# Kernel optimization log

Measured on AMD Instinct MI355X. Metric: run time of the kernel, lower is better.

## Reference

```python
import jax, jax.numpy as jnp
import numpy as np

V, E, H, L, S, B, FE = 50257, 768, 12, 4, 1024, 2, 4
HD = E // H
EPS = 1e-5


def setup_inputs() -> dict:
    key = jax.random.key(0)
    ks = jax.random.split(key, 16)
    def n(k, shape, scale=0.02):
        return jax.random.normal(k, shape, jnp.float32) * scale
    x = jax.random.randint(ks[0], (B, S), 0, V)
    mask = jnp.tril(jnp.ones((S, S), jnp.int32))[None, None]  # (1,1,S,S) causal
    return {
        "x": x,
        "mask": mask,
        "embed_W": n(ks[1], (V, E)),
        "pos_embed": n(ks[2], (1, S, E)),
        "fc_out_W": n(ks[3], (L, E, E)),
        "fc_out_b": jnp.zeros((L, E), jnp.float32),
        "gate_W": n(ks[4], (L, E, E)),
        "gate_b": jnp.zeros((L, E), jnp.float32),
        "ln1_g": jnp.ones((L, E), jnp.float32),
        "ln1_b": jnp.zeros((L, E), jnp.float32),
        "ln2_g": jnp.ones((L, E), jnp.float32),
        "ln2_b": jnp.zeros((L, E), jnp.float32),
        "ff1_W": n(ks[5], (L, E, FE * E)),
        "ff1_b": jnp.zeros((L, FE * E), jnp.float32),
        "ff2_W": n(ks[6], (L, FE * E, E)),
        "ff2_b": jnp.zeros((L, E), jnp.float32),
        "lnf_g": jnp.ones((E,), jnp.float32),
        "lnf_b": jnp.zeros((E,), jnp.float32),
        "head_W": n(ks[7], (E, V)),
    }


def _layernorm(y, g, b):
    m = jnp.mean(y, -1, keepdims=True)
    v = jnp.mean((y - m) ** 2, -1, keepdims=True)
    return (y - m) * jax.lax.rsqrt(v + EPS) * g + b


def reference(x, mask, embed_W, pos_embed, fc_out_W, fc_out_b, gate_W, gate_b,
              ln1_g, ln1_b, ln2_g, ln2_b, ff1_W, ff1_b, ff2_W, ff2_b,
              lnf_g, lnf_b, head_W):
    h = embed_W[x] + pos_embed[:, :x.shape[1], :]  # (B,S,E)
    scale = 1.0 / np.sqrt(HD)
    for i in range(L):
        # NOTE: source never applies the q/k/v Linear layers; heads are split directly.
        q = h.reshape(B, S, H, HD).transpose(0, 2, 1, 3)  # (B,H,S,HD)
        energy = jnp.einsum('bhqd,bhkd->bhqk', q, q)
        energy = jnp.where(mask == 0, jnp.float32(-1e20), energy)
        attn = jax.nn.softmax(energy * scale, axis=-1)
        o = jnp.einsum('bhqk,bhkd->bhqd', attn, q)
        o = o.transpose(0, 2, 1, 3).reshape(B, S, E)
        o = o @ fc_out_W[i] + fc_out_b[i]
        gate = jax.nn.sigmoid(jnp.mean(h, 1, keepdims=True) @ gate_W[i] + gate_b[i])
        h = _layernorm(gate * o + h, ln1_g[i], ln1_b[i])
        ff = jax.nn.gelu(h @ ff1_W[i] + ff1_b[i], approximate=False) @ ff2_W[i] + ff2_b[i]
        h = _layernorm(ff + h, ln2_g[i], ln2_b[i])
    h = _layernorm(h, lnf_g, lnf_b)
    logits = h @ head_W  # (B,S,V)
    return logits
```

## Files before the change

### kernel.cpp

```cpp
#include <hip/hip_runtime.h>
#include <hip/hip_bf16.h>

#define V 50257
#define E 768
#define NH 12
#define NL 4
#define SS 1024
#define BB 2
#define FEE 4
#define HD 64
#define EPSL 1e-5f
#define NPADH 50432

typedef __hip_bfloat16 bf16;
typedef __attribute__((ext_vector_type(8))) short short8;
typedef __attribute__((ext_vector_type(4))) float f32x4;
typedef __attribute__((ext_vector_type(4), aligned(4))) float f32x4a;

#define GLD_SRC(p) (const __attribute__((address_space(1))) void*)(p)
#define GLD_DST(p) (__attribute__((address_space(3))) void*)(p)

__device__ __forceinline__ float b2f(bf16 x){ return __bfloat162float(x); }

__global__ __launch_bounds__(256) void embed_kernel(const int* __restrict__ x, const float* __restrict__ eW,
                                                    const float* __restrict__ pos, bf16* __restrict__ hb){
  size_t i = (size_t)blockIdx.x*256 + threadIdx.x;
  if (i >= (size_t)BB*SS*E) return;
  int e = (int)(i % E);
  size_t bs = i / E;
  int s = (int)(bs % SS);
  int tok = x[bs];
  hb[i] = __float2bfloat16(eW[(size_t)tok*E + e] + pos[(size_t)s*E + e]);
}

__global__ __launch_bounds__(256) void cvt_attn(const bf16* __restrict__ hb, bf16* __restrict__ vT){
  __shared__ short t[64][65];
  int bid = blockIdx.x;
  int st = bid & 15, hh = (bid >> 4) % NH, b = bid / (16*NH);
  int s0 = st*64;
  int c = threadIdx.x & 63, rr = threadIdx.x >> 6;
  #pragma unroll
  for (int i = 0; i < 16; ++i){
    int r = rr*16 + i;
    t[r][c] = __builtin_bit_cast(short, hb[(size_t)(b*SS + s0 + r)*E + hh*HD + c]);
  }
  __syncthreads();
  #pragma unroll
  for (int i = 0; i < 16; ++i){
    int d = rr*16 + i;
    vT[(size_t)((b*NH + hh)*HD + d)*SS + s0 + c] = __builtin_bit_cast(bf16, t[c][d]);
  }
}

__global__ __launch_bounds__(256) void attn_mfma(const bf16* __restrict__ hb, const bf16* __restrict__ vT,
                                                 bf16* __restrict__ Ab){
  __shared__ short Qs[64*64];
  __shared__ short Ks[128*64];
  __shared__ short Vs[64*128];
  __shared__ short Ps[4][16*128];
  int tid = threadIdx.x, wave = tid >> 6, lane = tid & 63;
  int bid = blockIdx.x;
  int qt = 15 - (bid & 15);
  int hh = (bid >> 4) % NH, b = bid / (16*NH);
  int q0 = qt*64;
  int l15 = lane & 15, l4 = lane >> 4;
  int sw7 = l15 & 7;

  #pragma unroll
  for (int rnd = 0; rnd < 2; ++rnd){
    int o = rnd*256 + tid; int row = o >> 3; int cs = (((o & 7) ^ (row & 7))*8);
    __builtin_amdgcn_global_load_lds(GLD_SRC(hb + ((size_t)(b*SS + q0 + row)*E + hh*HD + cs)),
                                     GLD_DST(Qs + o*8), 16, 0, 0);
  }

  float mrun[4], lrun[4];
  #pragma unroll
  for (int j = 0; j < 4; ++j){ mrun[j] = -1e30f; lrun[j] = 0.f; }
  f32x4 acco[4] = {};

  int nkt = (qt >> 1) + 1;
  for (int kt = 0; kt < nkt; ++kt){
    int k0 = kt*128;
    __syncthreads();
    #pragma unroll
    for (int rnd = 0; rnd < 4; ++rnd){
      int o = rnd*256 + tid; int row = o >> 3; int cs = (((o & 7) ^ (row & 7))*8);
      __builtin_amdgcn_global_load_lds(GLD_SRC(hb + ((size_t)(b*SS + k0 + row)*E + hh*HD + cs)),
                                       GLD_DST(Ks + o*8), 16, 0, 0);
    }
    #pragma unroll
    for (int rnd = 0; rnd < 4; ++rnd){
      int o = rnd*256 + tid; int row = o >> 4; int cs = (((o & 15) ^ (row & 15))*8);
      __builtin_amdgcn_global_load_lds(GLD_SRC(vT + ((size_t)((b*NH + hh)*HD + row)*SS + k0 + cs)),
                                       GLD_DST(Vs + o*8), 16, 0, 0);
    }
    __syncthreads();

    f32x4 s[8] = {};
    __builtin_amdgcn_s_setprio(1);
    #pragma unroll
    for (int kk = 0; kk < 2; ++kk){
      int slot = kk*4 + l4;
      short8 af = *(const short8*)&Qs[(wave*16 + l15)*64 + ((slot ^ sw7)*8)];
      #pragma unroll
      for (int n = 0; n < 8; ++n){
        short8 bf8 = *(const short8*)&Ks[(n*16 + l15)*64 + ((slot ^ sw7)*8)];
        s[n] = __builtin_amdgcn_mfma_f32_16x16x32_bf16(af, bf8, s[n], 0, 0, 0);
      }
    }
    __builtin_amdgcn_s_setprio(0);

    bool diag = (kt == nkt - 1);
    #pragma unroll
    for (int j = 0; j < 4; ++j){
      int qg = q0 + wave*16 + l4*4 + j;
      float tmax = -1e30f;
      #pragma unroll
      for (int n = 0; n < 8; ++n){
        float v = s[n][j]*0.125f;
        if (diag && (k0 + n*16 + l15) > qg) v = -1e30f;
        s[n][j] = v; tmax = fmaxf(tmax, v);
      }
      tmax = fmaxf(tmax, __shfl_xor(tmax, 1, 64));
      tmax = fmaxf(tmax, __shfl_xor(tmax, 2, 64));
      tmax = fmaxf(tmax, __shfl_xor(tmax, 4, 64));
      tmax = fmaxf(tmax, __shfl_xor(tmax, 8, 64));
      float mnew = fmaxf(mrun[j], tmax);
      float alpha = __expf(mrun[j] - mnew);
      float rsum = 0.f;
      #pragma unroll
      for (int n = 0; n < 8; ++n){
        float p = __expf(s[n][j] - mnew);
        s[n][j] = p; rsum += p;
      }
      rsum += __shfl_xor(rsum, 1, 64);
      rsum += __shfl_xor(rsum, 2, 64);
      rsum += __shfl_xor(rsum, 4, 64);
      rsum += __shfl_xor(rsum, 8, 64);
      lrun[j] = lrun[j]*alpha + rsum;
      mrun[j] = mnew;
      #pragma unroll
      for (int n = 0; n < 4; ++n) acco[n][j] *= alpha;
      int prow = l4*4 + j;
      #pragma unroll
      for (int n = 0; n < 8; ++n){
        bf16 hv = __float2bfloat16(s[n][j]);
        int slot = (n*2 + (l15 >> 3)) ^ prow;
        Ps[wave][prow*128 + slot*8 + (l15 & 7)] = __builtin_bit_cast(short, hv);
      }
    }
    __syncthreads();

    __builtin_amdgcn_s_setprio(1);
    #pragma unroll
    for (int kk = 0; kk < 4; ++kk){
      int slot = kk*4 + l4;
      short8 pa = *(const short8*)&Ps[wave][l15*128 + ((slot ^ l15)*8)];
      #pragma unroll
      for (int n = 0; n < 4; ++n){
        short8 vb = *(const short8*)&Vs[(n*16 + l15)*128 + ((slot ^ l15)*8)];
        acco[n] = __builtin_amdgcn_mfma_f32_16x16x32_bf16(pa, vb, acco[n], 0, 0, 0);
      }
    }
    __builtin_amdgcn_s_setprio(0);
  }

  #pragma unroll
  for (int j = 0; j < 4; ++j){
    float inv = 1.f / lrun[j];
    int qg = q0 + wave*16 + l4*4 + j;
    #pragma unroll
    for (int n = 0; n < 4; ++n){
      Ab[(size_t)(b*SS + qg)*E + hh*HD + n*16 + l15] = __float2bfloat16(acco[n][j]*inv);
    }
  }
}

__global__ __launch_bounds__(256) void hmean1_kernel(const bf16* __restrict__ hb, float* __restrict__ ph){
  int bid = blockIdx.x;
  int ec = bid % 3, tc = (bid/3) & 15, b = bid / 48;
  int e = ec*256 + threadIdx.x;
  float s = 0.f;
  #pragma unroll 8
  for (int t = tc*64; t < tc*64 + 64; ++t) s += b2f(hb[((size_t)b*SS + t)*E + e]);
  ph[((size_t)b*16 + tc)*E + e] = s;
}

__global__ __launch_bounds__(256) void gate1_kernel(const float* __restrict__ ph, const float* __restrict__ gW,
                                                    float* __restrict__ pg){
  int bid = blockIdx.x;
  int ec = bid % 3, kc = (bid/3) & 3, b = bid / 12;
  int nn = ec*256 + threadIdx.x;
  __shared__ float hms[192];
  if (threadIdx.x < 192){
    int k = kc*192 + threadIdx.x;
    float s = 0.f;
    #pragma unroll
    for (int tc = 0; tc < 16; ++tc) s += ph[((size_t)b*16 + tc)*E + k];
    hms[threadIdx.x] = s * (1.0f/SS);
  }
  __syncthreads();
  float acc = 0.f;
  #pragma unroll 8
  for (int j = 0; j < 192; ++j) acc += hms[j] * gW[(size_t)(kc*192 + j)*E + nn];
  pg[((size_t)b*4 + kc)*E + nn] = acc;
}

__global__ __launch_bounds__(256) void wcvt_kernel(const float* __restrict__ W, bf16* __restrict__ Wt,
                                                   int K, int N, int Npad){
  int l = blockIdx.z;
  W  += (size_t)l*K*N;
  Wt += (size_t)l*Npad*K;
  __shared__ float t[32][33];
  int n0 = blockIdx.x*32, k0 = blockIdx.y*32;
  int tx = threadIdx.x & 31, ty8 = threadIdx.x >> 5;
  #pragma unroll
  for (int i = 0; i < 4; ++i){
    int k = k0 + ty8 + i*8, n = n0 + tx;
    t[ty8 + i*8][tx] = (k < K && n < N) ? W[(size_t)k*N + n] : 0.f;
  }
  __syncthreads();
  #pragma unroll
  for (int i = 0; i < 4; ++i){
    int n = n0 + ty8 + i*8, k = k0 + tx;
    if (n < Npad && k < K) Wt[(size_t)n*K + k] = __float2bfloat16(t[tx][ty8 + i*8]);
  }
}

template<int EPI>
__global__ __launch_bounds__(256, 2) void mfma_gemm(const bf16* __restrict__ A, const bf16* __restrict__ Bt,
                                                    const float* __restrict__ bias, void* __restrict__ Cv,
                                                    int M, int N, int Kslice, int Ktot){
  __shared__ short As[2][128*64];
  __shared__ short Bs[2][128*64];
  int tid = threadIdx.x;
  int wave = tid >> 6, lane = tid & 63;
  int wr = wave >> 1, wc = wave & 1;
  int l15 = lane & 15, l4 = lane >> 4;
  int sw7 = l15 & 7;
  int n0 = blockIdx.x * 128, m0 = blockIdx.y * 128;
  size_t koff = (size_t)blockIdx.z * Kslice;
  f32x4 acc[4][4] = {};
  int srow = tid >> 3;
  int sj = tid & 7;
  const int nks = Kslice >> 6;

  #define STAGE128(bsel, kt) do {                                              \
    int kb = (kt)*64;                                                          \
    _Pragma("unroll")                                                          \
    for (int iss = 0; iss < 4; ++iss){                                         \
      int r = srow + iss*32;                                                   \
      int cs = ((sj ^ (r & 7))*8);                                             \
      __builtin_amdgcn_global_load_lds(GLD_SRC(A + (size_t)(m0 + r)*Ktot + koff + kb + cs),  \
                                       GLD_DST(&As[bsel][r*64 + sj*8]), 16, 0, 0);           \
      __builtin_amdgcn_global_load_lds(GLD_SRC(Bt + (size_t)(n0 + r)*Ktot + koff + kb + cs), \
                                       GLD_DST(&Bs[bsel][r*64 + sj*8]), 16, 0, 0);           \
    }                                                                          \
  } while(0)

  STAGE128(0, 0);
  for (int kt = 0; kt < nks; ++kt){
    int cur = kt & 1;
    if (kt + 1 < nks){
      STAGE128(cur ^ 1, kt + 1);
      asm volatile("s_waitcnt vmcnt(8)" ::: "memory");
    } else {
      asm volatile("s_waitcnt vmcnt(0)" ::: "memory");
    }
    __builtin_amdgcn_s_barrier();
    __builtin_amdgcn_sched_barrier(0);
    __builtin_amdgcn_s_setprio(1);
    #pragma unroll
    for (int kk = 0; kk < 2; ++kk){
      int slot = kk*4 + l4;
      short8 af[4], bfr[4];
      #pragma unroll
      for (int m = 0; m < 4; ++m)
        af[m] = *(const short8*)&As[cur][(wr*64 + m*16 + l15)*64 + ((slot ^ sw7)*8)];
      #pragma unroll
      for (int n = 0; n < 4; ++n)
        bfr[n] = *(const short8*)&Bs[cur][(wc*64 + n*16 + l15)*64 + ((slot ^ sw7)*8)];
      #pragma unroll
      for (int m = 0; m < 4; ++m)
        #pragma unroll
        for (int n = 0; n < 4; ++n)
          acc[m][n] = __builtin_amdgcn_mfma_f32_16x16x32_bf16(af[m], bfr[n], acc[m][n], 0, 0, 0);
    }
    __builtin_amdgcn_s_setprio(0);
    __builtin_amdgcn_s_barrier();
    __builtin_amdgcn_sched_barrier(0);
  }
  #undef STAGE128

  if (EPI == 3){
    int lrow = l4*4;
    #pragma unroll
    for (int m = 0; m < 4; ++m){
      int row = m0 + wr*64 + m*16 + lrow;
      #pragma unroll
      for (int n = 0; n < 4; ++n){
        int col = n0 + wc*64 + n*16 + l15;
        if (col >= N) continue;
        #pragma unroll
        for (int j = 0; j < 4; ++j){
          float v = acc[m][n][j] + bias[col];
          v = 0.5f*v*(1.0f + erff(v*0.70710678f));
          ((bf16*)Cv)[(size_t)(row + j)*N + col] = __float2bfloat16(v);
        }
      }
    }
  } else {
    __syncthreads();
    float* Cf = (float*)Cv + (size_t)blockIdx.z * M * N;
    float* sw = ((float*)&As[0][0]) + wave*1104;
    int rbase = m0 + wr*64;
    int c0w = n0 + wc*64;
    #pragma unroll
    for (int m = 0; m < 4; ++m){
      #pragma unroll
      for (int n = 0; n < 4; ++n)
        #pragma unroll
        for (int j = 0; j < 4; ++j)
          sw[(l4*4 + j)*68 + n*16 + l15] = acc[m][n][j];
      #pragma unroll
      for (int jj = 0; jj < 4; ++jj){
        int rl = jj*4 + l4;
        f32x4a v = *(const f32x4a*)&sw[rl*68 + l15*4];
        int row = rbase + m*16 + rl;
        int col = c0w + l15*4;
        if (col + 3 < N){
          *(f32x4a*)&Cf[(size_t)row*N + col] = v;
        } else {
          #pragma unroll
          for (int c = 0; c < 4; ++c) if (col + c < N) Cf[(size_t)row*N + col + c] = v[c];
        }
      }
    }
  }
}

__global__ __launch_bounds__(512, 2) void gemm256(const bf16* __restrict__ A, const bf16* __restrict__ Bt,
                                                  float* __restrict__ C, int M, int N, int K, int MT){
  __shared__ short As[2][256*64];
  __shared__ short Bs[2][256*64];
  int tid = threadIdx.x;
  int wave = tid >> 6, lane = tid & 63;
  int wr = wave >> 2, wc = wave & 3;
  int l15 = lane & 15, l4 = lane >> 4;
  int sw7 = l15 & 7;

  int lid = blockIdx.x;
  int cpx = gridDim.x >> 3;
  int wg = (lid & 7)*cpx + (lid >> 3);
  int m0 = (wg % MT)*256, n0 = (wg / MT)*256;

  int srow = tid >> 3;
  int sj = tid & 7;
  const int nks = K >> 6;

  #define STAGE256(bsel, kt) do {                                             \
    int kb = (kt)*64;                                                         \
    _Pragma("unroll")                                                         \
    for (int rnd = 0; rnd < 4; ++rnd){                                        \
      int r = rnd*64 + srow;                                                  \
      int cs = ((sj ^ (r & 7))*8);                                            \
      __builtin_amdgcn_global_load_lds(GLD_SRC(A + (size_t)(m0 + r)*K + kb + cs),   \
                                       GLD_DST(&As[bsel][r*64 + sj*8]), 16, 0, 0);  \
      __builtin_amdgcn_global_load_lds(GLD_SRC(Bt + (size_t)(n0 + r)*K + kb + cs),  \
                                       GLD_DST(&Bs[bsel][r*64 + sj*8]), 16, 0, 0);  \
    }                                                                         \
  } while(0)

  f32x4 acc[8][4] = {};
  STAGE256(0, 0);
  for (int kt = 0; kt < nks; ++kt){
    int cur = kt & 1;
    if (kt + 1 < nks){
      STAGE256(cur ^ 1, kt + 1);
      asm volatile("s_waitcnt vmcnt(8)" ::: "memory");
    } else {
      asm volatile("s_waitcnt vmcnt(0)" ::: "memory");
    }
    __builtin_amdgcn_s_barrier();
    __builtin_amdgcn_sched_barrier(0);
    __builtin_amdgcn_s_setprio(1);
    #pragma unroll
    for (int kk = 0; kk < 2; ++kk){
      int slot = kk*4 + l4;
      short8 af[8], bfr[4];
      #pragma unroll
      for (int m = 0; m < 8; ++m)
        af[m] = *(const short8*)&As[cur][(wr*128 + m*16 + l15)*64 + ((slot ^ sw7)*8)];
      #pragma unroll
      for (int n = 0; n < 4; ++n)
        bfr[n] = *(const short8*)&Bs[cur][(wc*64 + n*16 + l15)*64 + ((slot ^ sw7)*8)];
      #pragma unroll
      for (int m = 0; m < 8; ++m)
        #pragma unroll
        for (int n = 0; n < 4; ++n)
          acc[m][n] = __builtin_amdgcn_mfma_f32_16x16x32_bf16(af[m], bfr[n], acc[m][n], 0, 0, 0);
    }
    __builtin_amdgcn_s_setprio(0);
    __builtin_amdgcn_s_barrier();
    __builtin_amdgcn_sched_barrier(0);
  }
  #undef STAGE256

  __syncthreads();
  float* sw = ((float*)&As[0][0]) + wave*1104;
  int rbase = m0 + wr*128;
  int c0w = n0 + wc*64;
  #pragma unroll
  for (int m = 0; m < 8; ++m){
    #pragma unroll
    for (int n = 0; n < 4; ++n)
      #pragma unroll
      for (int j = 0; j < 4; ++j)
        sw[(l4*4 + j)*68 + n*16 + l15] = acc[m][n][j];
    #pragma unroll
    for (int jj = 0; jj < 4; ++jj){
      int rl = jj*4 + l4;
      f32x4a v = *(const f32x4a*)&sw[rl*68 + l15*4];
      int row = rbase + m*16 + rl;
      int col = c0w + l15*4;
      if (col + 3 < N){
        *(f32x4a*)&C[(size_t)row*N + col] = v;
      } else {
        #pragma unroll
        for (int c = 0; c < 4; ++c) if (col + c < N) C[(size_t)row*N + col + c] = v[c];
      }
    }
  }
}

__global__ __launch_bounds__(256) void ln_kernel(const float* __restrict__ parts, int np,
                                                 const float* __restrict__ bias,
                                                 const bf16* __restrict__ residb,
                                                 const float* __restrict__ pg, const float* __restrict__ gb,
                                                 const float* __restrict__ g, const float* __restrict__ bta,
                                                 bf16* __restrict__ outb){
  const size_t PS = (size_t)BB*SS*E;
  int row = blockIdx.x;
  int b = row >> 10;
  int tid = threadIdx.x;
  __shared__ float sred[4];
  float y[3];
  float lsum = 0.f;
  #pragma unroll
  for (int i = 0; i < 3; ++i){
    int e = tid + i*256;
    float v = bias ? bias[e] : 0.f;
    for (int p = 0; p < np; ++p) v += parts[(size_t)p*PS + (size_t)row*E + e];
    if (pg){
      float ga = pg[(size_t)(b*4+0)*E + e] + pg[(size_t)(b*4+1)*E + e]
               + pg[(size_t)(b*4+2)*E + e] + pg[(size_t)(b*4+3)*E + e] + gb[e];
      v *= 1.0f / (1.0f + __expf(-ga));
    }
    if (residb) v += b2f(residb[(size_t)row*E + e]);
    y[i] = v; lsum += v;
  }
  for (int off = 32; off > 0; off >>= 1) lsum += __shfl_down(lsum, off, 64);
  int wid = tid >> 6, lane = tid & 63;
  if (lane == 0) sred[wid] = lsum;
  __syncthreads();
  float mean = (sred[0]+sred[1]+sred[2]+sred[3]) * (1.0f/E);
  __syncthreads();
  float lvar = 0.f;
  #pragma unroll
  for (int i = 0; i < 3; ++i){ float d = y[i]-mean; lvar += d*d; }
  for (int off = 32; off > 0; off >>= 1) lvar += __shfl_down(lvar, off, 64);
  if (lane == 0) sred[wid] = lvar;
  __syncthreads();
  float rstd = rsqrtf((sred[0]+sred[1]+sred[2]+sred[3]) * (1.0f/E) + EPSL);
  __syncthreads();
  #pragma unroll
  for (int i = 0; i < 3; ++i){
    int e = tid + i*256;
    outb[(size_t)row*E + e] = __float2bfloat16((y[i]-mean)*rstd*g[e] + bta[e]);
  }
}

extern "C" void kernel_launch(void* const* d_in, const int* in_sizes, int n_in,
                              void* d_out, int out_size, void* d_ws, size_t ws_size,
                              hipStream_t stream) {
  const int*   x      = (const int*)  d_in[0];
  const float* embedW = (const float*)d_in[2];
  const float* pos    = (const float*)d_in[3];
  const float* fcW    = (const float*)d_in[4];
  const float* fcB    = (const float*)d_in[5];
  const float* gW     = (const float*)d_in[6];
  const float* gB     = (const float*)d_in[7];
  const float* ln1g   = (const float*)d_in[8];
  const float* ln1b   = (const float*)d_in[9];
  const float* ln2g   = (const float*)d_in[10];
  const float* ln2b   = (const float*)d_in[11];
  const float* f1W    = (const float*)d_in[12];
  const float* f1B    = (const float*)d_in[13];
  const float* f2W    = (const float*)d_in[14];
  const float* f2B    = (const float*)d_in[15];
  const float* lnfg   = (const float*)d_in[16];
  const float* lnfb   = (const float*)d_in[17];
  const float* headW  = (const float*)d_in[18];
  float* out = (float*)d_out;

  const size_t BSE = (size_t)BB*SS*E;
  float* o    = (float*)d_ws;
  float* tmp  = o   + BSE;
  float* ph   = tmp + 2*BSE;
  float* pg   = ph  + (size_t)BB*16*E;
  bf16* abA   = (bf16*)(pg + (size_t)BB*4*E);
  bf16* abF   = abA + BSE;
  bf16* WfcT  = abF + BSE*FEE;
  bf16* Wf1T  = WfcT + (size_t)NL*E*E;
  bf16* Wf2T  = Wf1T + (size_t)NL*FEE*E*E;
  bf16* WheadT= Wf2T + (size_t)NL*FEE*E*E;
  bf16* hb    = (bf16*)o;
  bf16* vT    = hb + BSE;

  const int rows = BB*SS;

  embed_kernel<<<(int)((BSE + 255)/256), 256, 0, stream>>>(x, embedW, pos, hb);

  { dim3 g(E/32, E/32, NL);        wcvt_kernel<<<g, 256, 0, stream>>>(fcW, WfcT, E, E, E); }
  { dim3 g((FEE*E)/32, E/32, NL);  wcvt_kernel<<<g, 256, 0, stream>>>(f1W, Wf1T, E, FEE*E, FEE*E); }
  { dim3 g(E/32, (FEE*E)/32, NL);  wcvt_kernel<<<g, 256, 0, stream>>>(f2W, Wf2T, FEE*E, E, E); }
  { dim3 g(NPADH/32, E/32, 1);     wcvt_kernel<<<g, 256, 0, stream>>>(headW, WheadT, E, V, NPADH); }

  for (int l = 0; l < NL; ++l){
    size_t oEE = (size_t)l*E*E, oE = (size_t)l*E, oFb = (size_t)l*FEE*E;

    hmean1_kernel<<<BB*16*3, 256, 0, stream>>>(hb, ph);
    gate1_kernel<<<BB*4*3, 256, 0, stream>>>(ph, gW + oEE, pg);

    cvt_attn<<<BB*NH*16, 256, 0, stream>>>(hb, vT);
    attn_mfma<<<BB*NH*16, 256, 0, stream>>>(hb, vT, abA);

    { dim3 g(E/128, rows/128, 2);
      mfma_gemm<0><<<g, 256, 0, stream>>>(abA, WfcT + oEE, nullptr, tmp, rows, E, E/2, E); }

    ln_kernel<<<rows, 256, 0, stream>>>(tmp, 2, fcB + oE, hb, pg, gB + oE,
                                        ln1g + oE, ln1b + oE, abA);

    { dim3 g((FEE*E)/128, rows/128, 1);
      mfma_gemm<3><<<g, 256, 0, stream>>>(abA, Wf1T + (size_t)l*FEE*E*E, f1B + oFb, abF, rows, FEE*E, E, E); }

    { dim3 g(E/128, rows/128, 2);
      mfma_gemm<0><<<g, 256, 0, stream>>>(abF, Wf2T + (size_t)l*FEE*E*E, nullptr, tmp, rows, E, FEE*E/2, FEE*E); }

    ln_kernel<<<rows, 256, 0, stream>>>(tmp, 2, f2B + oE, abA, nullptr, nullptr,
                                        ln2g + oE, ln2b + oE, hb);
  }

  ln_kernel<<<rows, 256, 0, stream>>>(nullptr, 0, nullptr, hb, nullptr, nullptr,
                                      lnfg, lnfb, abA);
  {
    gemm256<<<(rows/256)*(NPADH/256), 512, 0, stream>>>(abA, WheadT, out, rows, V, E, rows/256);
  }
}
```

Baseline: 1.003 ms.

## Halve gemm256 K-tile to 32 and raise occupancy target to four blocks

Shrinks the gemm256 K-step from 64 to 32, which halves the shared-memory staging buffers. It rewrites the load distribution and XOR swizzle for the 32-wide rows and lowers the vmcnt wait threshold to match. The launch-bounds minimum block count rises from 2 to 4 so more workgroups can be resident and hide latency. In exchange there are twice as many barriers per K, and the tighter register budget could force spills of the 128-float accumulator.

Measured after the change: 2.143 ms. +113.6%, slower.

```diff
diff --git a/kernel.cpp b/kernel.cpp
--- a/kernel.cpp
+++ b/kernel.cpp
@@ -339,61 +339,60 @@
   }
 }
 
-__global__ __launch_bounds__(512, 2) void gemm256(const bf16* __restrict__ A, const bf16* __restrict__ Bt,
+__global__ __launch_bounds__(512, 4) void gemm256(const bf16* __restrict__ A, const bf16* __restrict__ Bt,
                                                   float* __restrict__ C, int M, int N, int K, int MT){
-  __shared__ short As[2][256*64];
-  __shared__ short Bs[2][256*64];
+  __shared__ short As[2][256*32];
+  __shared__ short Bs[2][256*32];
   int tid = threadIdx.x;
   int wave = tid >> 6, lane = tid & 63;
   int wr = wave >> 2, wc = wave & 3;
   int l15 = lane & 15, l4 = lane >> 4;
-  int sw7 = l15 & 7;
 
   int lid = blockIdx.x;
   int cpx = gridDim.x >> 3;
   int wg = (lid & 7)*cpx + (lid >> 3);
   int m0 = (wg % MT)*256, n0 = (wg / MT)*256;
 
-  int srow = tid >> 3;
-  int sj = tid & 7;
-  const int nks = K >> 6;
-
-  #define STAGE256(bsel, kt) do {                                             \
-    int kb = (kt)*64;                                                         \
-    _Pragma("unroll")                                                         \
-    for (int rnd = 0; rnd < 4; ++rnd){                                        \
-      int r = rnd*64 + srow;                                                  \
-      int cs = ((sj ^ (r & 7))*8);                                            \
-      __builtin_amdgcn_global_load_lds(GLD_SRC(A + (size_t)(m0 + r)*K + kb + cs),   \
-                                       GLD_DST(&As[bsel][r*64 + sj*8]), 16, 0, 0);  \
-      __builtin_amdgcn_global_load_lds(GLD_SRC(Bt + (size_t)(n0 + r)*K + kb + cs),  \
-                                       GLD_DST(&Bs[bsel][r*64 + sj*8]), 16, 0, 0);  \
-    }                                                                         \
+  const int nks = K >> 5;
+
+  #define STG32(bsel, kt) do {                                                        \
+    int kb = (kt)*32;                                                                 \
+    _Pragma("unroll")                                                                 \
+    for (int i = 0; i < 2; ++i){                                                      \
+      int o = i*512 + tid; int r = o >> 2; int sl = o & 3;                            \
+      int cs = ((sl ^ ((r >> 1) & 3))*8);                                             \
+      __builtin_amdgcn_global_load_lds(GLD_SRC(A + (size_t)(m0 + r)*K + kb + cs),     \
+                                       GLD_DST(&As[bsel][r*32 + sl*8]), 16, 0, 0);    \
+      __builtin_amdgcn_global_load_lds(GLD_SRC(Bt + (size_t)(n0 + r)*K + kb + cs),    \
+                                       GLD_DST(&Bs[bsel][r*32 + sl*8]), 16, 0, 0);    \
+    }                                                                                 \
   } while(0)
 
   f32x4 acc[8][4] = {};
-  STAGE256(0, 0);
+  STG32(0, 0);
   for (int kt = 0; kt < nks; ++kt){
     int cur = kt & 1;
     if (kt + 1 < nks){
-      STAGE256(cur ^ 1, kt + 1);
-      asm volatile("s_waitcnt vmcnt(8)" ::: "memory");
+      STG32(cur ^ 1, kt + 1);
+      asm volatile("s_waitcnt vmcnt(4)" ::: "memory");
     } else {
       asm volatile("s_waitcnt vmcnt(0)" ::: "memory");
     }
     __builtin_amdgcn_s_barrier();
     __builtin_amdgcn_sched_barrier(0);
     __builtin_amdgcn_s_setprio(1);
-    #pragma unroll
-    for (int kk = 0; kk < 2; ++kk){
-      int slot = kk*4 + l4;
+    {
       short8 af[8], bfr[4];
       #pragma unroll
-      for (int m = 0; m < 8; ++m)
-        af[m] = *(const short8*)&As[cur][(wr*128 + m*16 + l15)*64 + ((slot ^ sw7)*8)];
-      #pragma unroll
-      for (int n = 0; n < 4; ++n)
-        bfr[n] = *(const short8*)&Bs[cur][(wc*64 + n*16 + l15)*64 + ((slot ^ sw7)*8)];
+      for (int m = 0; m < 8; ++m){
+        int row = wr*128 + m*16 + l15;
+        af[m] = *(const short8*)&As[cur][row*32 + ((l4 ^ ((row >> 1) & 3))*8)];
+      }
+      #pragma unroll
+      for (int n = 0; n < 4; ++n){
+        int row = wc*64 + n*16 + l15;
+        bfr[n] = *(const short8*)&Bs[cur][row*32 + ((l4 ^ ((row >> 1) & 3))*8)];
+      }
       #pragma unroll
       for (int m = 0; m < 8; ++m)
         #pragma unroll
@@ -404,7 +403,7 @@
     __builtin_amdgcn_s_barrier();
     __builtin_amdgcn_sched_barrier(0);
   }
-  #undef STAGE256
+  #undef STG32
 
   __syncthreads();
   float* sw = ((float*)&As[0][0]) + wave*1104;
```
